# Optimization experiments

Hardware: AMD Instinct MI355X
Metric: run time of the kernel (lower is better)

The kernel has to match this reference:

```python
import jax, jax.numpy as jnp
import numpy as np

N = 50000      # nodes
E = 800000     # edges (avg degree 16)
IN = 128       # in_feats
OUT = 128      # out_feats
ASSIGN = 256   # assign_dim = B graphs * 8 clusters
B = 32         # batch_size (num graphs)


def setup_inputs() -> dict:
    key = jax.random.key(0)
    k0, k1, k2, k3 = jax.random.split(key, 4)
    x = jax.random.normal(k0, (N, IN), jnp.float32)
    edge_index = jax.random.randint(k1, (2, E), 0, N, dtype=jnp.int32)
    # sorted graph ids, ~equal-sized graphs (mirrors block_diag mask construction)
    batch = ((jnp.arange(N, dtype=jnp.int32) * B) // N).astype(jnp.int32)
    # SAGEConv params: Linear(2*in_feats -> out) on concat([x, mean_neigh])
    W_embed = jax.random.normal(k2, (2 * IN, OUT), jnp.float32) / np.float32(np.sqrt(2 * IN))
    b_embed = jnp.zeros((OUT,), jnp.float32)
    W_pool = jax.random.normal(k3, (2 * IN, ASSIGN), jnp.float32) / np.float32(np.sqrt(2 * IN))
    b_pool = jnp.zeros((ASSIGN,), jnp.float32)
    return dict(x=x, edge_index=edge_index, batch=batch,
                W_embed=W_embed, b_embed=b_embed, W_pool=W_pool, b_pool=b_pool)


def _sage(x, src, dst, W, b):
    # mean aggregation over in-neighbors (messages src -> dst), then Linear on concat
    n = x.shape[0]
    deg = jax.ops.segment_sum(jnp.ones((src.shape[0],), x.dtype), dst, num_segments=n)
    neigh = jax.ops.segment_sum(x[src], dst, num_segments=n) / jnp.maximum(deg, 1.0)[:, None]
    return jnp.concatenate([x, neigh], axis=-1) @ W + b


def reference(x, edge_index, batch, W_embed, b_embed, W_pool, b_pool):
    src, dst = edge_index[0], edge_index[1]
    embed = _sage(x, src, dst, W_embed, b_embed)                      # [N, OUT]
    pooled = jax.nn.softmax(_sage(x, src, dst, W_pool, b_pool), -1)   # [N, ASSIGN]
    # block-diagonal mask: node i of graph g sees columns [g*C, (g+1)*C)
    C = ASSIGN // B
    cols = jnp.arange(ASSIGN, dtype=batch.dtype) // C
    mask = (batch[:, None] == cols[None, :]).astype(x.dtype)          # [N, ASSIGN]
    # NOTE: faithful to original: softmax of (mask * pooled), zeros contribute exp(0)
    r = jax.nn.softmax(mask * pooled, axis=-1) * mask
    r = r / (r.sum(axis=-1, keepdims=True) + 1e-13)                   # [N, ASSIGN]
    h = r.T @ embed                                                   # [ASSIGN, OUT]
    # adj_new = S^T A S with A sparse COO (rows=edge_index[0], cols=edge_index[1])
    ar = jax.ops.segment_sum(r[dst], src, num_segments=x.shape[0])    # A @ S : [N, ASSIGN]
    adj_new = r.T @ ar                                                # [ASSIGN, ASSIGN]
    return (adj_new, h)
```

## Files before the change

kernel.cpp:

```cpp
#include <hip/hip_runtime.h>
#include <hip/hip_bf16.h>

#define N_ 50000
#define E_ 800000
#define IN_ 128
#define OUT_ 128
#define ASSIGN_ 256
#define B_ 32
#define KTOT 256
#define JTOT 384
#define HCHUNK 32
#define ACHUNK 32
#define AST 72
#define NXP ((N_ + 127) / 128)
#define NGB (NXP * 3)
#define NCVX 6250

#define NBKT 128
#define NPB 391
#define BCAP 7000
#define EPB 4096
#define NBLK_A ((E_ + EPB - 1) / EPB)
#define NPRE (NBLK_A + NCVX + 384)

typedef __attribute__((ext_vector_type(8))) short short8;
typedef __attribute__((ext_vector_type(4))) float f32x4;
typedef __attribute__((ext_vector_type(2))) float f32x2;
typedef __attribute__((ext_vector_type(4))) unsigned short ushort4v;
typedef __attribute__((ext_vector_type(2))) unsigned short ushort2v;
typedef unsigned short u16;

__device__ inline unsigned short f2bf(float v) {
    union { float f; unsigned u; } a;
    a.f = v;
    unsigned r = a.u + 0x7fff + ((a.u >> 16) & 1);
    return (unsigned short)(r >> 16);
}
__device__ inline float bf2f(unsigned short b) {
    union { unsigned u; float f; } a;
    a.u = ((unsigned)b) << 16;
    return a.f;
}

__device__ inline unsigned enc8(float v) {
    union { float f; unsigned u; } a;
    a.f = v * 0x1p-120f;
    unsigned b = a.u;
    unsigned r = b + 0x7FFFF + ((b >> 20) & 1);
    return ((r >> 20) & 0x7F) | ((b >> 24) & 0x80);
}
__device__ inline float2 dec8x2(unsigned short p) {
#if defined(__has_builtin) && __has_builtin(__builtin_amdgcn_cvt_pk_f32_fp8)
    f32x2 r = __builtin_amdgcn_cvt_pk_f32_fp8((int)(unsigned)p, false);
    return make_float2(r.x, r.y);
#else
    unsigned u0 = p & 0xffu, u1 = (p >> 8) & 0xffu;
    union { unsigned u; float f; } a, b;
    a.u = ((u0 & 0x80u) << 24) | ((u0 & 0x7fu) << 20);
    b.u = ((u1 & 0x80u) << 24) | ((u1 & 0x7fu) << 20);
    return make_float2(a.f * 0x1p+120f, b.f * 0x1p+120f);
#endif
}

__global__ __launch_bounds__(256) void k_pre(const int* __restrict__ ei,
                                             int* __restrict__ bktFill,
                                             int2* __restrict__ ebkt,
                                             const float* __restrict__ x,
                                             unsigned short* __restrict__ xhi,
                                             unsigned char* __restrict__ xq,
                                             const float* __restrict__ We,
                                             const float* __restrict__ be,
                                             const float* __restrict__ Wp,
                                             const float* __restrict__ bp,
                                             unsigned short* __restrict__ WThi,
                                             float* __restrict__ bias) {
    __shared__ int lh[NBKT], lbase[NBKT], lofs[NBKT];
    int bid = blockIdx.x;
    int t = threadIdx.x;
    if (bid < NBLK_A) {
        int e0 = bid * EPB;
        if (t < NBKT) { lh[t] = 0; lofs[t] = 0; }
        __syncthreads();
        int ss[16], dd[16];
#pragma unroll
        for (int i = 0; i < 16; i++) {
            int e = e0 + i * 256 + t;
            ss[i] = 0; dd[i] = -1;
            if (e < E_) {
                ss[i] = ei[e];
                dd[i] = ei[E_ + e];
                atomicAdd(&lh[dd[i] / NPB], 1);
            }
        }
        __syncthreads();
        if (t < NBKT) lbase[t] = t * BCAP + atomicAdd(&bktFill[t], lh[t]);
        __syncthreads();
#pragma unroll
        for (int i = 0; i < 16; i++) {
            if (dd[i] >= 0) {
                int b = dd[i] / NPB;
                int o = atomicAdd(&lofs[b], 1);
                ebkt[lbase[b] + o] = make_int2(ss[i], dd[i]);
            }
        }
        return;
    }
    if (bid >= NBLK_A + NCVX) {
        int idx = (bid - NBLK_A - NCVX) * 256 + t;
        if (idx < JTOT * KTOT) {
            int j = idx / KTOT, k = idx - j * KTOT;
            float v = (j < 128) ? We[k * 128 + j] : Wp[k * 256 + (j - 128)];
            WThi[idx] = f2bf(v);
        }
        if (idx < JTOT) bias[idx] = (idx < 128) ? be[idx] : bp[idx - 128];
        return;
    }
    int i4 = ((bid - NBLK_A) * 256 + t) * 4;
    if (i4 >= N_ * 128) return;
    float4 v = *(const float4*)(x + i4);
    ushort4v h;
    h.x = f2bf(v.x); h.y = f2bf(v.y); h.z = f2bf(v.z); h.w = f2bf(v.w);
    *(ushort4v*)(xhi + i4) = h;
    unsigned q = enc8(v.x) | (enc8(v.y) << 8) | (enc8(v.z) << 16) | (enc8(v.w) << 24);
    *(unsigned*)(xq + i4) = q;
}

__global__ __launch_bounds__(256) void k_binB(const int* __restrict__ bktFill,
                                              const int2* __restrict__ ebkt,
                                              int* __restrict__ ready,
                                              int* __restrict__ rowStart,
                                              int* __restrict__ csr_src,
                                              int* __restrict__ csr_dst) {
    __shared__ int ldeg[NPB];
    __shared__ int lscan[512];
    __shared__ int bsc[NBKT];
    __shared__ int lfill[NPB];
    int b = blockIdx.x, t = threadIdx.x;
    for (int i = t; i < NPB; i += 256) ldeg[i] = 0;
    __syncthreads();
    int base = b * BCAP;
    int cnt = bktFill[b];
    int n0 = b * NPB;
    for (int j = t; j < cnt; j += 256)
        atomicAdd(&ldeg[ebkt[base + j].y - n0], 1);
    __syncthreads();
    lscan[t] = (t < NPB) ? ldeg[t] : 0;
    lscan[t + 256] = (t + 256 < NPB) ? ldeg[t + 256] : 0;
    __syncthreads();
    for (int off = 1; off < 512; off <<= 1) {
        int x0 = lscan[t];
        int x1 = lscan[t + 256];
        int a0 = (t >= off) ? lscan[t - off] : 0;
        int a1 = (t + 256 >= off) ? lscan[t + 256 - off] : 0;
        __syncthreads();
        lscan[t] = x0 + a0;
        lscan[t + 256] = x1 + a1;
        __syncthreads();
    }
    if (t == 0) atomicExch(&ready[b], lscan[NPB - 1] + 1);
    if (t < NBKT) {
        int v;
        while ((v = atomicAdd(&ready[t], 0)) == 0) __builtin_amdgcn_s_sleep(8);
        bsc[t] = v - 1;
    }
    __syncthreads();
    for (int off = 1; off < NBKT; off <<= 1) {
        int x = (t < NBKT) ? bsc[t] : 0;
        int add = (t < NBKT && t >= off) ? bsc[t - off] : 0;
        __syncthreads();
        if (t < NBKT) bsc[t] = x + add;
        __syncthreads();
    }
    int base0 = (b == 0) ? 0 : bsc[b - 1];
    for (int i = t; i < NPB; i += 256) {
        int n = n0 + i;
        if (n < N_) {
            int excl = (i == 0) ? 0 : lscan[i - 1];
            lfill[i] = excl;
            rowStart[n] = base0 + excl;
        }
    }
    __syncthreads();
    for (int j = t; j < cnt; j += 256) {
        int2 sd = ebkt[base + j];
        int p = base0 + atomicAdd(&lfill[sd.y - n0], 1);
        csr_src[p] = sd.x;
        csr_dst[p] = sd.y;
    }
    if (b == 0 && t == 0) rowStart[N_] = E_;
}

__global__ __launch_bounds__(256) void k_agg(const unsigned char* __restrict__ xq,
                                             const int* __restrict__ rowStart,
                                             const int* __restrict__ csr_src,
                                             unsigned short* __restrict__ nhi) {
    int node = blockIdx.x * 4 + (threadIdx.x >> 6);
    if (node >= N_) return;
    int lane = threadIdx.x & 63;
    int es = lane >> 3;
    int fb = lane & 7;
    int a = rowStart[node], bnd = rowStart[node + 1];
    float acc[16];
#pragma unroll
    for (int k = 0; k < 16; k++) acc[k] = 0.f;
#define DEC(Q)                                                       \
    {                                                                \
        unsigned wq[4] = {(Q).x, (Q).y, (Q).z, (Q).w};               \
        _Pragma("unroll")                                            \
        for (int wi = 0; wi < 4; wi++) {                             \
            float2 f01 = dec8x2((unsigned short)(wq[wi] & 0xffffu)); \
            float2 f23 = dec8x2((unsigned short)(wq[wi] >> 16));     \
            acc[wi * 4 + 0] += f01.x; acc[wi * 4 + 1] += f01.y;      \
            acc[wi * 4 + 2] += f23.x; acc[wi * 4 + 3] += f23.y;      \
        }                                                            \
    }
    int j = a;
    for (; j + 8 < bnd; j += 16) {
        int s0 = csr_src[j + es];
        uint4 q0 = *(const uint4*)(xq + (size_t)s0 * 128 + fb * 16);
        uint4 q1 = {0, 0, 0, 0};
        int e1 = j + 8 + es;
        if (e1 < bnd) {
            int s1 = csr_src[e1];
            q1 = *(const uint4*)(xq + (size_t)s1 * 128 + fb * 16);
        }
        DEC(q0);
        DEC(q1);
    }
    if (j < bnd) {
        uint4 q0 = {0, 0, 0, 0};
        int e0 = j + es;
        if (e0 < bnd) {
            int s0 = csr_src[e0];
            q0 = *(const uint4*)(xq + (size_t)s0 * 128 + fb * 16);
        }
        DEC(q0);
    }
#undef DEC
#pragma unroll
    for (int k = 0; k < 16; k++) {
        acc[k] += __shfl_xor(acc[k], 8, 64);
        acc[k] += __shfl_xor(acc[k], 16, 64);
        acc[k] += __shfl_xor(acc[k], 32, 64);
    }
    float inv = 1.0f / (float)max(bnd - a, 1);
    if (es == 0) {
        short8 o0, o1;
#pragma unroll
        for (int k = 0; k < 8; k++) {
            o0[k] = (short)f2bf(acc[k] * inv);
            o1[k] = (short)f2bf(acc[k + 8] * inv);
        }
        *(short8*)(nhi + (size_t)node * 128 + fb * 16) = o0;
        *(short8*)(nhi + (size_t)node * 128 + fb * 16 + 8) = o1;
    }
}

#define LDA 40
__global__ __launch_bounds__(256) void k_gemm(const unsigned short* __restrict__ xhi,
                                              const unsigned short* __restrict__ nhi,
                                              const unsigned short* __restrict__ WThi,
                                              const float* __restrict__ bias,
                                              unsigned short* __restrict__ embed,
                                              unsigned short* __restrict__ plog) {
    __shared__ __align__(16) union {
        struct { u16 Ah[128][LDA]; u16 Bh[128][LDA]; } s;
        u16 ep[64 * 128];
    } sm;
    int t = threadIdx.x;
    int wave = t >> 6, lane = t & 63;
    int wm = wave >> 1, wn = wave & 1;
    int q = lane >> 4, lr = lane & 15;

    int id = blockIdx.x;
    int xi, cc;
    if (id < (NXP / 8) * 24) {
        xi = (id / 24) * 8 + (id & 7);
        cc = (id % 24) >> 3;
    } else {
        int r2 = id - (NXP / 8) * 24;
        xi = (NXP / 8) * 8 + r2 % (NXP % 8);
        cc = r2 / (NXP % 8);
    }
    int row0 = xi * 128;
    int col0 = cc * 128;

    f32x4 acc[4][4] = {};
    int smr = t >> 1;
    int kc = (t & 1) * 16;
    int node = row0 + smr;

    short8 vh0, vh1, wh0, wh1;
#define LOADK(KT)                                                                    \
    {                                                                                \
        const u16* Ah_src = ((KT) < 128) ? xhi : nhi;                                \
        int kb = ((KT) & 127) + kc;                                                  \
        vh0 = {}; vh1 = {};                                                          \
        if (node < N_) {                                                             \
            const short8* ph = (const short8*)(Ah_src + (size_t)node * 128 + kb);    \
            vh0 = ph[0]; vh1 = ph[1];                                                \
        }                                                                            \
        const short8* pw = (const short8*)(WThi + (size_t)(col0 + smr) * 256 + (KT) + kc); \
        wh0 = pw[0]; wh1 = pw[1];                                                    \
    }
    LOADK(0);
    for (int kt = 0; kt < KTOT; kt += 32) {
        *(short8*)&sm.s.Ah[smr][kc] = vh0;
        *(short8*)&sm.s.Ah[smr][kc + 8] = vh1;
        *(short8*)&sm.s.Bh[smr][kc] = wh0;
        *(short8*)&sm.s.Bh[smr][kc + 8] = wh1;
        __syncthreads();
        if (kt + 32 < KTOT) LOADK(kt + 32);

        short8 afh[4];
#pragma unroll
        for (int mi = 0; mi < 4; mi++) {
            int r = wm * 64 + mi * 16 + lr;
            afh[mi] = *(const short8*)&sm.s.Ah[r][q * 8];
        }
#pragma unroll
        for (int ni = 0; ni < 4; ni++) {
            int r = wn * 64 + ni * 16 + lr;
            short8 bfh = *(const short8*)&sm.s.Bh[r][q * 8];
#pragma unroll
            for (int mi = 0; mi < 4; mi++)
                acc[mi][ni] = __builtin_amdgcn_mfma_f32_16x16x32_bf16(afh[mi], bfh, acc[mi][ni], 0, 0, 0);
        }
        __syncthreads();
    }
#undef LOADK

    for (int half = 0; half < 2; half++) {
        __syncthreads();
        if (wm == half) {
#pragma unroll
            for (int mi = 0; mi < 4; mi++)
#pragma unroll
                for (int ni = 0; ni < 4; ni++) {
                    int lcol = wn * 64 + ni * 16 + lr;
                    float bj = bias[col0 + lcol];
#pragma unroll
                    for (int r = 0; r < 4; r++) {
                        int lrow = mi * 16 + q * 4 + r;
                        sm.ep[lrow * 128 + lcol] = f2bf(acc[mi][ni][r] + bj);
                    }
                }
        }
        __syncthreads();
#pragma unroll
        for (int i = 0; i < 4; i++) {
            int chunk = i * 256 + t;
            int lrow = chunk >> 4;
            int lco = (chunk & 15) * 8;
            int grow = row0 + half * 64 + lrow;
            if (grow < N_) {
                short8 v = *(const short8*)&sm.ep[lrow * 128 + lco];
                if (col0 < 128)
                    *(short8*)(embed + (size_t)grow * 128 + lco) = v;
                else
                    *(short8*)(plog + (size_t)grow * 256 + (col0 - 128) + lco) = v;
            }
        }
    }
}

__global__ __launch_bounds__(256) void k_r(const unsigned short* __restrict__ plog,
                                           const int* __restrict__ batch,
                                           float* __restrict__ r8,
                                           unsigned short* __restrict__ r8b) {
    int node = blockIdx.x * 4 + (threadIdx.x >> 6);
    int lane = threadIdx.x & 63;
    if (node >= N_) return;
    ushort4v p4 = *(const ushort4v*)(plog + (size_t)node * 256 + lane * 4);
    float px = bf2f(p4.x), py = bf2f(p4.y), pz = bf2f(p4.z), pw = bf2f(p4.w);
    float m = fmaxf(fmaxf(px, py), fmaxf(pz, pw));
    for (int off = 32; off; off >>= 1) m = fmaxf(m, __shfl_xor(m, off, 64));
    float s = expf(px - m) + expf(py - m) + expf(pz - m) + expf(pw - m);
    for (int off = 32; off; off >>= 1) s += __shfl_xor(s, off, 64);
    int g = batch[node];
    float v = 0.f;
    if (lane < 8) v = expf(bf2f(plog[(size_t)node * 256 + g * 8 + lane]) - m) / s;
    float M2 = v;
    for (int off = 4; off; off >>= 1) M2 = fmaxf(M2, __shfl_xor(M2, off, 64));
    float e = expf(v - M2);
    float Sg = e;
    for (int off = 4; off; off >>= 1) Sg += __shfl_xor(Sg, off, 64);
    float D2 = Sg + 248.0f * expf(-M2);
    float r = e / (Sg + 1e-13f * D2);
    if (lane < 8) {
        r8[node * 8 + lane] = r;
        r8b[node * 8 + lane] = f2bf(r);
    }
}

__global__ __launch_bounds__(256) void k_tail(const int* __restrict__ rowStart,
                                              const int* __restrict__ csr_src,
                                              const int* __restrict__ csr_dst,
                                              const unsigned short* __restrict__ r8b,
                                              float* __restrict__ partAdj,
                                              const unsigned short* __restrict__ embed,
                                              const float* __restrict__ r8,
                                              float* __restrict__ partH) {
    __shared__ __align__(16) unsigned short Ab[256 * AST];
    __shared__ __align__(16) unsigned short Bb[16 * AST];
    int id = blockIdx.x;
    int t = threadIdx.x;
    if (id >= B_ * ACHUNK) {
        int idh = id - B_ * ACHUNK;
        int g = idh & 31;
        int c = idh >> 5;
        int o = t & 127, half = t >> 7;
        int n0g = (g * N_ + 31) >> 5;
        int n1g = ((g + 1) * N_ + 31) >> 5;
        int len = n1g - n0g;
        int a = n0g + (len * c) / HCHUNK;
        int b = n0g + (len * (c + 1)) / HCHUNK;
        float a0 = 0.f, a1 = 0.f, a2 = 0.f, a3 = 0.f;
#pragma unroll 4
        for (int n = a; n < b; n++) {
            float e = bf2f(embed[(size_t)n * 128 + o]);
            const float* rr = r8 + n * 8 + half;
            a0 += rr[0] * e;
            a1 += rr[2] * e;
            a2 += rr[4] * e;
            a3 += rr[6] * e;
        }
        float* pb = partH + (g * HCHUNK + c) * 1024;
        pb[(half + 0) * 128 + o] = a0;
        pb[(half + 2) * 128 + o] = a1;
        pb[(half + 4) * 128 + o] = a2;
        pb[(half + 6) * 128 + o] = a3;
        return;
    }
    int gd = id & 31;
    int c = id >> 5;
    int wave = t >> 6, lane = t & 63;
    int q = lane >> 4, lr = lane & 15;
    int n0g = (gd * N_ + 31) >> 5;
    int n1g = ((gd + 1) * N_ + 31) >> 5;
    int len = n1g - n0g;
    int na = n0g + (len * c) / ACHUNK;
    int nb = n0g + (len * (c + 1)) / ACHUNK;
    int j0 = rowStart[na], j1 = rowStart[nb];

    uint4 z = {0, 0, 0, 0};
#pragma unroll
    for (int i = 0; i < 9; i++) *(uint4*)&Ab[(i * 256 + t) * 8] = z;
    if (t < 144) *(uint4*)&Bb[t * 8] = z;
    __syncthreads();

    f32x4 acc[4] = {};
    int el = t >> 2;
    int ap = t & 3;

    int jcur = j0 + el;
    unsigned sv = 0, dv = 0;
    int gs = 0;
    bool have = jcur < j1;
    if (have) {
        int s = csr_src[jcur];
        int d = csr_dst[jcur];
        gs = (s * B_) / N_;
        sv = *(const unsigned*)(r8b + (size_t)s * 8 + ap * 2);
        dv = *(const unsigned*)(r8b + (size_t)d * 8 + ap * 2);
    }
    int pca = -1;

    for (int jt = j0; jt < j1; jt += 64) {
        if (pca >= 0) {
            Ab[pca * AST + el] = 0;
            Ab[(pca + 1) * AST + el] = 0;
            Bb[(ap * 2) * AST + el] = 0;
            Bb[(ap * 2 + 1) * AST + el] = 0;
        }
        int ca = -1;
        if (have) {
            ca = gs * 8 + ap * 2;
            Ab[ca * AST + el] = (unsigned short)sv;
            Ab[(ca + 1) * AST + el] = (unsigned short)(sv >> 16);
            Bb[(ap * 2) * AST + el] = (unsigned short)dv;
            Bb[(ap * 2 + 1) * AST + el] = (unsigned short)(dv >> 16);
        }
        __syncthreads();
        int jn = jt + 64 + el;
        bool haveN = jn < j1;
        unsigned svN = 0, dvN = 0;
        int gsN = 0;
        if (haveN) {
            int s = csr_src[jn];
            int d = csr_dst[jn];
            gsN = (s * B_) / N_;
            svN = *(const unsigned*)(r8b + (size_t)s * 8 + ap * 2);
            dvN = *(const unsigned*)(r8b + (size_t)d * 8 + ap * 2);
        }
        short8 bf0 = *(const short8*)&Bb[lr * AST + q * 8];
        short8 bf1 = *(const short8*)&Bb[lr * AST + 32 + q * 8];
#pragma unroll
        for (int mi = 0; mi < 4; mi++) {
            int col = (wave * 4 + mi) * 16 + lr;
            short8 a0 = *(const short8*)&Ab[col * AST + q * 8];
            short8 a1 = *(const short8*)&Ab[col * AST + 32 + q * 8];
            acc[mi] = __builtin_amdgcn_mfma_f32_16x16x32_bf16(a0, bf0, acc[mi], 0, 0, 0);
            acc[mi] = __builtin_amdgcn_mfma_f32_16x16x32_bf16(a1, bf1, acc[mi], 0, 0, 0);
        }
        __syncthreads();
        pca = ca;
        have = haveN; gs = gsN; sv = svN; dv = dvN;
    }

    float* pb = partAdj + (gd * ACHUNK + c) * 2048;
    if (lr < 8) {
#pragma unroll
        for (int mi = 0; mi < 4; mi++) {
            int mbase = (wave * 4 + mi) * 16 + q * 4;
#pragma unroll
            for (int r = 0; r < 4; r++)
                pb[(mbase + r) * 8 + lr] = acc[mi][r];
        }
    }
}

__global__ __launch_bounds__(256) void k_red(const float* __restrict__ partAdj,
                                             const float* __restrict__ partH,
                                             float* __restrict__ out) {
    int o = blockIdx.x * 256 + threadIdx.x;
    if (o < 256 * 256) {
        int row = o >> 8, col = o & 255;
        int gd = col >> 3, b = col & 7;
        int li = row * 8 + b;
        float s = 0.f;
#pragma unroll
        for (int c = 0; c < ACHUNK; c++) s += partAdj[(gd * ACHUNK + c) * 2048 + li];
        out[o] = s;
    } else {
        int idx = o - 256 * 256;
        int g = idx >> 10;
        int local = idx & 1023;
        float s = 0.f;
#pragma unroll
        for (int c = 0; c < HCHUNK; c++) s += partH[(g * HCHUNK + c) * 1024 + local];
        out[256 * 256 + idx] = s;
    }
}

extern "C" void kernel_launch(void* const* d_in, const int* in_sizes, int n_in,
                              void* d_out, int out_size, void* d_ws, size_t ws_size,
                              hipStream_t stream) {
    const float* x = (const float*)d_in[0];
    const int* ei = (const int*)d_in[1];
    const int* batch = (const int*)d_in[2];
    const float* We = (const float*)d_in[3];
    const float* be = (const float*)d_in[4];
    const float* Wp = (const float*)d_in[5];
    const float* bp = (const float*)d_in[6];
    float* out = (float*)d_out;

    char* w = (char*)d_ws;
    auto alloc = [&](size_t bytes) -> char* {
        char* p = w;
        w += (bytes + 255) & ~(size_t)255;
        return p;
    };
    unsigned short* xhi = (unsigned short*)alloc((size_t)N_ * 128 * 2);
    unsigned char* xq = (unsigned char*)alloc((size_t)N_ * 128);
    unsigned short* nhi = (unsigned short*)alloc((size_t)N_ * 128 * 2);
    unsigned short* WThi = (unsigned short*)alloc((size_t)JTOT * KTOT * 2);
    unsigned short* embed = (unsigned short*)alloc((size_t)N_ * 128 * 2);
    unsigned short* plog = (unsigned short*)alloc((size_t)N_ * 256 * 2);
    float* r8 = (float*)alloc((size_t)N_ * 8 * 4);
    unsigned short* r8b = (unsigned short*)alloc((size_t)N_ * 8 * 2);
    float* bias = (float*)alloc(JTOT * 4);
    int* rowStart = (int*)alloc((size_t)(N_ + 1) * 4);
    int* csr_src = (int*)alloc((size_t)E_ * 4);
    int* csr_dst = (int*)alloc((size_t)E_ * 4);
    int* flags = (int*)alloc(2 * NBKT * 4);
    int* bktFill = flags;
    int* ready = flags + NBKT;
    int2* ebkt = (int2*)alloc((size_t)NBKT * BCAP * 8);
    float* partH = (float*)alloc((size_t)B_ * HCHUNK * 1024 * 4);
    float* partAdj = (float*)alloc((size_t)B_ * ACHUNK * 2048 * 4);

    hipMemsetAsync(flags, 0, 2 * NBKT * 4, stream);
    k_pre<<<NPRE, 256, 0, stream>>>(ei, bktFill, ebkt, x, xhi, xq, We, be, Wp, bp, WThi, bias);
    k_binB<<<NBKT, 256, 0, stream>>>(bktFill, ebkt, ready, rowStart, csr_src, csr_dst);
    k_agg<<<(N_ + 3) / 4, 256, 0, stream>>>(xq, rowStart, csr_src, nhi);
    k_gemm<<<NGB, 256, 0, stream>>>(xhi, nhi, WThi, bias, embed, plog);
    k_r<<<(N_ + 3) / 4, 256, 0, stream>>>(plog, batch, r8, r8b);
    k_tail<<<2 * B_ * ACHUNK, 256, 0, stream>>>(rowStart, csr_src, csr_dst, r8b, partAdj,
                                                embed, r8, partH);
    k_red<<<(256 * 256 + 256 * 128 + 255) / 256, 256, 0, stream>>>(partAdj, partH, out);
}
```

Baseline: 225.9 us.

## Fuse neighbor aggregation into GEMM with per-panel producer/consumer flags

Merges the aggregation kernel into the GEMM kernel. The first NXP blocks each aggregate neighbor features for their 128-row panel, write nhi with atomic stores, and then set a ready flag. The remaining blocks do the x-half of the K loop first and spin on that flag before loading the neighbor half. This is meant to overlap gather work with GEMM and remove one launch, but it relies on producer blocks being scheduled before consumers, which risks deadlock or spin stalls. Aggregation also becomes serialized per wave (32 nodes each) inside only NXP blocks, which lowers parallelism for the gather.

```diff
diff --git a/kernel.cpp b/kernel.cpp
--- a/kernel.cpp
+++ b/kernel.cpp
@@ -29,6 +29,7 @@
 typedef __attribute__((ext_vector_type(4))) unsigned short ushort4v;
 typedef __attribute__((ext_vector_type(2))) unsigned short ushort2v;
 typedef unsigned short u16;
+typedef unsigned long long u64;
 
 __device__ inline unsigned short f2bf(float v) {
     union { float f; unsigned u; } a;
@@ -190,79 +191,17 @@
     if (b == 0 && t == 0) rowStart[N_] = E_;
 }
 
-__global__ __launch_bounds__(256) void k_agg(const unsigned char* __restrict__ xq,
-                                             const int* __restrict__ rowStart,
-                                             const int* __restrict__ csr_src,
-                                             unsigned short* __restrict__ nhi) {
-    int node = blockIdx.x * 4 + (threadIdx.x >> 6);
-    if (node >= N_) return;
-    int lane = threadIdx.x & 63;
-    int es = lane >> 3;
-    int fb = lane & 7;
-    int a = rowStart[node], bnd = rowStart[node + 1];
-    float acc[16];
-#pragma unroll
-    for (int k = 0; k < 16; k++) acc[k] = 0.f;
-#define DEC(Q)                                                       \
-    {                                                                \
-        unsigned wq[4] = {(Q).x, (Q).y, (Q).z, (Q).w};               \
-        _Pragma("unroll")                                            \
-        for (int wi = 0; wi < 4; wi++) {                             \
-            float2 f01 = dec8x2((unsigned short)(wq[wi] & 0xffffu)); \
-            float2 f23 = dec8x2((unsigned short)(wq[wi] >> 16));     \
-            acc[wi * 4 + 0] += f01.x; acc[wi * 4 + 1] += f01.y;      \
-            acc[wi * 4 + 2] += f23.x; acc[wi * 4 + 3] += f23.y;      \
-        }                                                            \
-    }
-    int j = a;
-    for (; j + 8 < bnd; j += 16) {
-        int s0 = csr_src[j + es];
-        uint4 q0 = *(const uint4*)(xq + (size_t)s0 * 128 + fb * 16);
-        uint4 q1 = {0, 0, 0, 0};
-        int e1 = j + 8 + es;
-        if (e1 < bnd) {
-            int s1 = csr_src[e1];
-            q1 = *(const uint4*)(xq + (size_t)s1 * 128 + fb * 16);
-        }
-        DEC(q0);
-        DEC(q1);
-    }
-    if (j < bnd) {
-        uint4 q0 = {0, 0, 0, 0};
-        int e0 = j + es;
-        if (e0 < bnd) {
-            int s0 = csr_src[e0];
-            q0 = *(const uint4*)(xq + (size_t)s0 * 128 + fb * 16);
-        }
-        DEC(q0);
-    }
-#undef DEC
-#pragma unroll
-    for (int k = 0; k < 16; k++) {
-        acc[k] += __shfl_xor(acc[k], 8, 64);
-        acc[k] += __shfl_xor(acc[k], 16, 64);
-        acc[k] += __shfl_xor(acc[k], 32, 64);
-    }
-    float inv = 1.0f / (float)max(bnd - a, 1);
-    if (es == 0) {
-        short8 o0, o1;
-#pragma unroll
-        for (int k = 0; k < 8; k++) {
-            o0[k] = (short)f2bf(acc[k] * inv);
-            o1[k] = (short)f2bf(acc[k + 8] * inv);
-        }
-        *(short8*)(nhi + (size_t)node * 128 + fb * 16) = o0;
-        *(short8*)(nhi + (size_t)node * 128 + fb * 16 + 8) = o1;
-    }
-}
-
 #define LDA 40
-__global__ __launch_bounds__(256) void k_gemm(const unsigned short* __restrict__ xhi,
-                                              const unsigned short* __restrict__ nhi,
-                                              const unsigned short* __restrict__ WThi,
-                                              const float* __restrict__ bias,
-                                              unsigned short* __restrict__ embed,
-                                              unsigned short* __restrict__ plog) {
+__global__ __launch_bounds__(256) void k_ag(const unsigned char* __restrict__ xq,
+                                            const int* __restrict__ rowStart,
+                                            const int* __restrict__ csr_src,
+                                            unsigned short* __restrict__ nhi,
+                                            const unsigned short* __restrict__ xhi,
+                                            const unsigned short* __restrict__ WThi,
+                                            const float* __restrict__ bias,
+                                            unsigned short* __restrict__ embed,
+                                            unsigned short* __restrict__ plog,
+                                            int* __restrict__ panelReady) {
     __shared__ __align__(16) union {
         struct { u16 Ah[128][LDA]; u16 Bh[128][LDA]; } s;
         u16 ep[64 * 128];
@@ -271,19 +210,81 @@
     int wave = t >> 6, lane = t & 63;
     int wm = wave >> 1, wn = wave & 1;
     int q = lane >> 4, lr = lane & 15;
-
     int id = blockIdx.x;
+
     int xi, cc;
-    if (id < (NXP / 8) * 24) {
-        xi = (id / 24) * 8 + (id & 7);
-        cc = (id % 24) >> 3;
-    } else {
-        int r2 = id - (NXP / 8) * 24;
-        xi = (NXP / 8) * 8 + r2 % (NXP % 8);
-        cc = r2 / (NXP % 8);
-    }
+    bool producer = (id < NXP);
+    if (producer) { xi = id; cc = 0; }
+    else { int cid = id - NXP; xi = cid >> 1; cc = 1 + (cid & 1); }
     int row0 = xi * 128;
     int col0 = cc * 128;
+
+    if (producer) {
+        int es = lane >> 3;
+        int fb = lane & 7;
+        for (int nn = 0; nn < 32; nn++) {
+            int node = row0 + wave * 32 + nn;
+            if (node >= N_) break;
+            int a = rowStart[node], bnd = rowStart[node + 1];
+            float acc[16];
+#pragma unroll
+            for (int k = 0; k < 16; k++) acc[k] = 0.f;
+#define DEC(Q)                                                       \
+            {                                                        \
+                unsigned wq[4] = {(Q).x, (Q).y, (Q).z, (Q).w};       \
+                _Pragma("unroll")                                    \
+                for (int wi = 0; wi < 4; wi++) {                     \
+                    float2 f01 = dec8x2((unsigned short)(wq[wi] & 0xffffu)); \
+                    float2 f23 = dec8x2((unsigned short)(wq[wi] >> 16));     \
+                    acc[wi * 4 + 0] += f01.x; acc[wi * 4 + 1] += f01.y;      \
+                    acc[wi * 4 + 2] += f23.x; acc[wi * 4 + 3] += f23.y;      \
+                }                                                    \
+            }
+            int j = a;
+            for (; j + 8 < bnd; j += 16) {
+                int s0 = csr_src[j + es];
+                uint4 q0 = *(const uint4*)(xq + (size_t)s0 * 128 + fb * 16);
+                uint4 q1 = {0, 0, 0, 0};
+                int e1 = j + 8 + es;
+                if (e1 < bnd) {
+                    int s1 = csr_src[e1];
+                    q1 = *(const uint4*)(xq + (size_t)s1 * 128 + fb * 16);
+                }
+                DEC(q0);
+                DEC(q1);
+            }
+            if (j < bnd) {
+                uint4 q0 = {0, 0, 0, 0};
+                int e0 = j + es;
+                if (e0 < bnd) {
+                    int s0 = csr_src[e0];
+                    q0 = *(const uint4*)(xq + (size_t)s0 * 128 + fb * 16);
+                }
+                DEC(q0);
+            }
+#undef DEC
+#pragma unroll
+            for (int k = 0; k < 16; k++) {
+                acc[k] += __shfl_xor(acc[k], 8, 64);
+                acc[k] += __shfl_xor(acc[k], 16, 64);
+                acc[k] += __shfl_xor(acc[k], 32, 64);
+            }
+            float inv = 1.0f / (float)max(bnd - a, 1);
+            if (es == 0) {
+                u64* dst = (u64*)(nhi + (size_t)node * 128 + fb * 16);
+#pragma unroll
+                for (int k = 0; k < 4; k++) {
+                    u64 wv = (u64)f2bf(acc[4 * k + 0] * inv)
+                           | ((u64)f2bf(acc[4 * k + 1] * inv) << 16)
+                           | ((u64)f2bf(acc[4 * k + 2] * inv) << 32)
+                           | ((u64)f2bf(acc[4 * k + 3] * inv) << 48);
+                    __hip_atomic_store(dst + k, wv, __ATOMIC_RELAXED, __HIP_MEMORY_SCOPE_AGENT);
+                }
+            }
+        }
+        __syncthreads();
+        if (t == 0) atomicExch(&panelReady[xi], 1);
+    }
 
     f32x4 acc[4][4] = {};
     int smr = t >> 1;
@@ -310,7 +311,15 @@
         *(short8*)&sm.s.Bh[smr][kc] = wh0;
         *(short8*)&sm.s.Bh[smr][kc + 8] = wh1;
         __syncthreads();
-        if (kt + 32 < KTOT) LOADK(kt + 32);
+        if (kt + 32 < KTOT) {
+            if (!producer && kt + 32 == 128) {
+                if (t == 0) {
+                    while (atomicAdd(&panelReady[xi], 0) == 0) __builtin_amdgcn_s_sleep(32);
+                }
+                __syncthreads();
+            }
+            LOADK(kt + 32);
+        }
 
         short8 afh[4];
 #pragma unroll
@@ -573,18 +582,18 @@
     int* rowStart = (int*)alloc((size_t)(N_ + 1) * 4);
     int* csr_src = (int*)alloc((size_t)E_ * 4);
     int* csr_dst = (int*)alloc((size_t)E_ * 4);
-    int* flags = (int*)alloc(2 * NBKT * 4);
+    int* flags = (int*)alloc((2 * NBKT + NXP) * 4);
     int* bktFill = flags;
     int* ready = flags + NBKT;
+    int* panelReady = flags + 2 * NBKT;
     int2* ebkt = (int2*)alloc((size_t)NBKT * BCAP * 8);
     float* partH = (float*)alloc((size_t)B_ * HCHUNK * 1024 * 4);
     float* partAdj = (float*)alloc((size_t)B_ * ACHUNK * 2048 * 4);
 
-    hipMemsetAsync(flags, 0, 2 * NBKT * 4, stream);
+    hipMemsetAsync(flags, 0, (2 * NBKT + NXP) * 4, stream);
     k_pre<<<NPRE, 256, 0, stream>>>(ei, bktFill, ebkt, x, xhi, xq, We, be, Wp, bp, WThi, bias);
     k_binB<<<NBKT, 256, 0, stream>>>(bktFill, ebkt, ready, rowStart, csr_src, csr_dst);
-    k_agg<<<(N_ + 3) / 4, 256, 0, stream>>>(xq, rowStart, csr_src, nhi);
-    k_gemm<<<NGB, 256, 0, stream>>>(xhi, nhi, WThi, bias, embed, plog);
+    k_ag<<<NGB, 256, 0, stream>>>(xq, rowStart, csr_src, nhi, xhi, WThi, bias, embed, plog, panelReady);
     k_r<<<(N_ + 3) / 4, 256, 0, stream>>>(plog, batch, r8, r8b);
     k_tail<<<2 * B_ * ACHUNK, 256, 0, stream>>>(rowStart, csr_src, csr_dst, r8b, partAdj,
                                                 embed, r8, partH);
```

Result: slower. 269.7 us (+19.4%).

## Double edge buckets for binning and restructure h partial sums across waves

Applied to the files above, without the earlier changes.

Edge binning now uses 256 buckets of 196 nodes, so the bucket count equals the block size and the CSR build kernel gets more, smaller blocks with a single-element scan per thread. The h partial-sum path is restructured so each wave walks an interleaved subset of nodes. Each lane loads two bf16 embed values and vectorised r8 rows and accumulates all 8 clusters. The four wave results are then reduced through shared memory. This trades some register and LDS use for better memory coalescing and parallelism. The bucket capacity is cut to 4000, which could overflow on skewed inputs.

```diff
diff --git a/kernel.cpp b/kernel.cpp
--- a/kernel.cpp
+++ b/kernel.cpp
@@ -16,9 +16,9 @@
 #define NGB (NXP * 3)
 #define NCVX 6250
 
-#define NBKT 128
-#define NPB 391
-#define BCAP 7000
+#define NBKT 256
+#define NPB 196
+#define BCAP 4000
 #define EPB 4096
 #define NBLK_A ((E_ + EPB - 1) / EPB)
 #define NPRE (NBLK_A + NCVX + 384)
@@ -79,7 +79,7 @@
     int t = threadIdx.x;
     if (bid < NBLK_A) {
         int e0 = bid * EPB;
-        if (t < NBKT) { lh[t] = 0; lofs[t] = 0; }
+        lh[t] = 0; lofs[t] = 0;
         __syncthreads();
         int ss[16], dd[16];
 #pragma unroll
@@ -93,7 +93,7 @@
             }
         }
         __syncthreads();
-        if (t < NBKT) lbase[t] = t * BCAP + atomicAdd(&bktFill[t], lh[t]);
+        lbase[t] = t * BCAP + atomicAdd(&bktFill[t], lh[t]);
         __syncthreads();
 #pragma unroll
         for (int i = 0; i < 16; i++) {
@@ -132,11 +132,11 @@
                                               int* __restrict__ csr_src,
                                               int* __restrict__ csr_dst) {
     __shared__ int ldeg[NPB];
-    __shared__ int lscan[512];
+    __shared__ int lscan[256];
     __shared__ int bsc[NBKT];
     __shared__ int lfill[NPB];
     int b = blockIdx.x, t = threadIdx.x;
-    for (int i = t; i < NPB; i += 256) ldeg[i] = 0;
+    if (t < NPB) ldeg[t] = 0;
     __syncthreads();
     int base = b * BCAP;
     int cnt = bktFill[b];
@@ -145,38 +145,34 @@
         atomicAdd(&ldeg[ebkt[base + j].y - n0], 1);
     __syncthreads();
     lscan[t] = (t < NPB) ? ldeg[t] : 0;
-    lscan[t + 256] = (t + 256 < NPB) ? ldeg[t + 256] : 0;
     __syncthreads();
-    for (int off = 1; off < 512; off <<= 1) {
+    for (int off = 1; off < 256; off <<= 1) {
         int x0 = lscan[t];
-        int x1 = lscan[t + 256];
         int a0 = (t >= off) ? lscan[t - off] : 0;
-        int a1 = (t + 256 >= off) ? lscan[t + 256 - off] : 0;
         __syncthreads();
         lscan[t] = x0 + a0;
-        lscan[t + 256] = x1 + a1;
         __syncthreads();
     }
     if (t == 0) atomicExch(&ready[b], lscan[NPB - 1] + 1);
-    if (t < NBKT) {
+    {
         int v;
         while ((v = atomicAdd(&ready[t], 0)) == 0) __builtin_amdgcn_s_sleep(8);
         bsc[t] = v - 1;
     }
     __syncthreads();
     for (int off = 1; off < NBKT; off <<= 1) {
-        int x = (t < NBKT) ? bsc[t] : 0;
-        int add = (t < NBKT && t >= off) ? bsc[t - off] : 0;
-        __syncthreads();
-        if (t < NBKT) bsc[t] = x + add;
+        int x = bsc[t];
+        int add = (t >= off) ? bsc[t - off] : 0;
+        __syncthreads();
+        bsc[t] = x + add;
         __syncthreads();
     }
     int base0 = (b == 0) ? 0 : bsc[b - 1];
-    for (int i = t; i < NPB; i += 256) {
-        int n = n0 + i;
+    if (t < NPB) {
+        int n = n0 + t;
         if (n < N_) {
-            int excl = (i == 0) ? 0 : lscan[i - 1];
-            lfill[i] = excl;
+            int excl = (t == 0) ? 0 : lscan[t - 1];
+            lfill[t] = excl;
             rowStart[n] = base0 + excl;
         }
     }
@@ -409,27 +405,35 @@
         int idh = id - B_ * ACHUNK;
         int g = idh & 31;
         int c = idh >> 5;
-        int o = t & 127, half = t >> 7;
+        int wv = t >> 6, l = t & 63;
         int n0g = (g * N_ + 31) >> 5;
         int n1g = ((g + 1) * N_ + 31) >> 5;
         int len = n1g - n0g;
         int a = n0g + (len * c) / HCHUNK;
         int b = n0g + (len * (c + 1)) / HCHUNK;
-        float a0 = 0.f, a1 = 0.f, a2 = 0.f, a3 = 0.f;
-#pragma unroll 4
-        for (int n = a; n < b; n++) {
-            float e = bf2f(embed[(size_t)n * 128 + o]);
-            const float* rr = r8 + n * 8 + half;
-            a0 += rr[0] * e;
-            a1 += rr[2] * e;
-            a2 += rr[4] * e;
-            a3 += rr[6] * e;
-        }
+        float acc[8][2] = {};
+        for (int n = a + wv; n < b; n += 4) {
+            unsigned e2 = *(const unsigned*)(embed + (size_t)n * 128 + l * 2);
+            float e0 = bf2f((u16)(e2 & 0xffffu));
+            float e1 = bf2f((u16)(e2 >> 16));
+            f32x4 r0 = *(const f32x4*)(r8 + n * 8);
+            f32x4 r1 = *(const f32x4*)(r8 + n * 8 + 4);
+#pragma unroll
+            for (int c2 = 0; c2 < 4; c2++) {
+                acc[c2][0] += r0[c2] * e0; acc[c2][1] += r0[c2] * e1;
+                acc[c2 + 4][0] += r1[c2] * e0; acc[c2 + 4][1] += r1[c2] * e1;
+            }
+        }
+        float* hredf = (float*)Ab;
+#pragma unroll
+        for (int c2 = 0; c2 < 8; c2++) {
+            hredf[wv * 1024 + c2 * 128 + l * 2] = acc[c2][0];
+            hredf[wv * 1024 + c2 * 128 + l * 2 + 1] = acc[c2][1];
+        }
+        __syncthreads();
         float* pb = partH + (g * HCHUNK + c) * 1024;
-        pb[(half + 0) * 128 + o] = a0;
-        pb[(half + 2) * 128 + o] = a1;
-        pb[(half + 4) * 128 + o] = a2;
-        pb[(half + 6) * 128 + o] = a3;
+        for (int o = t; o < 1024; o += 256)
+            pb[o] = (hredf[o] + hredf[1024 + o]) + (hredf[2048 + o] + hredf[3072 + o]);
         return;
     }
     int gd = id & 31;
```

Measured after the change: 218.0 us. 3.5% less time.
